# Performance work log

Measured on AMD Instinct MI355X. Metric: run time of the kernel, lower is better.

The kernel has to match this reference:

```python
import jax, jax.numpy as jnp
import numpy as np

N_NODES = 10000
N_EDGES = 160000
F_IN, D1, D2, D_OUT, K = 512, 512, 512, 256, 3


def _gcn_layer(x, row, col, w, W, b, n):
    # PyG GCNConv (improved=False): add self-loops with weight 1, sym norm.
    loop = jnp.arange(n)
    r = jnp.concatenate([row, loop])
    c = jnp.concatenate([col, loop])
    ww = jnp.concatenate([w, jnp.ones((n,), w.dtype)])
    deg = jax.ops.segment_sum(ww, c, num_segments=n)
    dinv = jnp.where(deg > 0, jax.lax.rsqrt(deg), 0.0)
    norm = dinv[r] * ww * dinv[c]              # [E+N]
    h = x @ W                                  # dense GEMM first (as PyG lin)
    out = jax.ops.segment_sum(norm[:, None] * h[r], c, num_segments=n)
    return out + b


def _cheb_layer(x, row, col, w, Wk, b, n):
    # PyG ChebConv, normalization='sym', lambda_max=2.0:
    # L_hat = 2L/lmax - I = -D^{-1/2} A D^{-1/2} (self-loops removed first).
    w0 = jnp.where(row == col, jnp.zeros((), w.dtype), w)  # remove self loops
    deg = jax.ops.segment_sum(w0, row, num_segments=n)
    dinv = jnp.where(deg > 0, jax.lax.rsqrt(deg), 0.0)
    norm = dinv[row] * w0 * dinv[col]          # [E]

    def lhat(z):  # L_hat @ z
        return -jax.ops.segment_sum(norm[:, None] * z[row], col, num_segments=n)

    Tx0 = x
    out = Tx0 @ Wk[0]
    Tx1 = lhat(x)
    out = out + Tx1 @ Wk[1]
    for k in range(2, Wk.shape[0]):            # static K, fine to unroll
        Tx2 = 2.0 * lhat(Tx1) - Tx0
        out = out + Tx2 @ Wk[k]
        Tx0, Tx1 = Tx1, Tx2
    return out + b


def setup_inputs() -> dict:
    key = jax.random.key(0)
    ks = jax.random.split(key, 9)
    x = jax.random.normal(ks[0], (N_NODES, F_IN), dtype=jnp.float32)
    edge_index = jax.random.randint(ks[1], (2, N_EDGES), 0, N_NODES, dtype=jnp.int64)
    edge_weight = jax.random.uniform(ks[2], (N_EDGES,), dtype=jnp.float32)
    s = lambda fan: 1.0 / np.sqrt(fan)
    W1 = jax.random.normal(ks[3], (F_IN, D1), dtype=jnp.float32) * s(F_IN)
    b1 = jnp.zeros((D1,), jnp.float32)
    W2 = jax.random.normal(ks[4], (D1, D2), dtype=jnp.float32) * s(D1)
    b2 = jnp.zeros((D2,), jnp.float32)
    Wc = jax.random.normal(ks[5], (K, D2, D_OUT), dtype=jnp.float32) * s(D2)
    bc = jnp.zeros((D_OUT,), jnp.float32)
    return {"x": x, "edge_index": edge_index, "edge_weight": edge_weight,
            "W1": W1, "b1": b1, "W2": W2, "b2": b2, "Wc": Wc, "bc": bc}


def reference(x, edge_index, edge_weight, W1, b1, W2, b2, Wc, bc):
    row, col = edge_index[0], edge_index[1]
    n = x.shape[0]
    h = jax.nn.celu(_gcn_layer(x, row, col, edge_weight, W1, b1, n))
    h = jax.nn.celu(_gcn_layer(h, row, col, edge_weight, W2, b2, n))
    h = jax.nn.celu(_cheb_layer(h, row, col, edge_weight, Wc, bc, n))
    return h
```

## Files before the change

kernel.cpp:

```cpp
#include <hip/hip_runtime.h>
#include <math.h>

#define N_NODES 10000
#define N_EDGES 160000
#define FDIM    512
#define DOUT    256
#define NCAT    768

typedef unsigned short ushort_t;
typedef unsigned int   uint_t;
typedef __attribute__((ext_vector_type(8))) short bf16x8;
typedef __attribute__((ext_vector_type(4))) float f32x4;

__device__ inline ushort_t f2bf(float f) {
    uint_t u = __float_as_uint(f);
    u += 0x7fffu + ((u >> 16) & 1u);
    return (ushort_t)(u >> 16);
}
__device__ inline void bf2f8(uint4 u, float* v) {
    v[0] = __uint_as_float(u.x << 16); v[1] = __uint_as_float(u.x & 0xffff0000u);
    v[2] = __uint_as_float(u.y << 16); v[3] = __uint_as_float(u.y & 0xffff0000u);
    v[4] = __uint_as_float(u.z << 16); v[5] = __uint_as_float(u.z & 0xffff0000u);
    v[6] = __uint_as_float(u.w << 16); v[7] = __uint_as_float(u.w & 0xffff0000u);
}
__device__ inline uint4 f2bf8v(const float* v) {
    uint4 u;
    u.x = (uint_t)f2bf(v[0]) | ((uint_t)f2bf(v[1]) << 16);
    u.y = (uint_t)f2bf(v[2]) | ((uint_t)f2bf(v[3]) << 16);
    u.z = (uint_t)f2bf(v[4]) | ((uint_t)f2bf(v[5]) << 16);
    u.w = (uint_t)f2bf(v[6]) | ((uint_t)f2bf(v[7]) << 16);
    return u;
}
__device__ inline void gld_lds16(const ushort_t* g, ushort_t* l) {
    __builtin_amdgcn_global_load_lds(
        (const __attribute__((address_space(1))) unsigned int*)g,
        (__attribute__((address_space(3))) unsigned int*)l,
        16, 0, 0);
}

#define EDGE_BLOCKS 625
#define XB_BLOCKS   5000

__global__ __launch_bounds__(256) void k_pre1(
    const int* __restrict__ row, const int* __restrict__ col,
    const float* __restrict__ w,
    float* deg_g, float* deg_c, int* counts,
    const float* __restrict__ x,  ushort_t* __restrict__ xb,
    const float* __restrict__ W1, ushort_t* __restrict__ W1t,
    const float* __restrict__ W2, ushort_t* __restrict__ W2t,
    const float* __restrict__ Wc, ushort_t* __restrict__ Wcatt)
{
    __shared__ float tile[64][65];
    int b = blockIdx.x;
    int tid = threadIdx.x;
    if (b < EDGE_BLOCKS) {
        int e = b * 256 + tid;
        if (e < N_EDGES) {
            int r = row[e], c = col[e];
            float wv = w[e];
            atomicAdd(&deg_g[c], wv);
            if (r != c) atomicAdd(&deg_c[r], wv);
            atomicAdd(&counts[c], 1);
        }
        return;
    }
    b -= EDGE_BLOCKS;
    if (b < XB_BLOCKS) {
        int t = b * 256 + tid;
        float4 v = *(const float4*)(x + (size_t)t * 4);
        uint2 p;
        p.x = (uint_t)f2bf(v.x) | ((uint_t)f2bf(v.y) << 16);
        p.y = (uint_t)f2bf(v.z) | ((uint_t)f2bf(v.w) << 16);
        *(uint2*)(xb + (size_t)t * 4) = p;
        return;
    }
    b -= XB_BLOCKS;
    const float* src; const float* src2 = nullptr;
    ushort_t* dst; int kt, ntG, srcld;
    if (b < 64) {
        kt = b >> 3; ntG = b & 7; srcld = FDIM;
        src = W1 + (size_t)(kt * 64) * FDIM + ntG * 64;
        dst = W1t;
    } else if (b < 128) {
        int bb = b - 64;
        kt = bb >> 3; ntG = bb & 7; srcld = FDIM;
        src = W2 + (size_t)(kt * 64) * FDIM + ntG * 64;
        dst = W2t;
    } else {
        int bb = b - 128;
        ntG = bb / 8; kt = bb % 8; srcld = DOUT;
        int s = ntG >> 2;
        int nl = (ntG & 3) * 64;
        if (s == 0) {
            src  = Wc + (size_t)(kt * 64) * DOUT + nl;
            src2 = Wc + (size_t)2 * FDIM * DOUT + (size_t)(kt * 64) * DOUT + nl;
        } else if (s == 1) {
            src  = Wc + (size_t)1 * FDIM * DOUT + (size_t)(kt * 64) * DOUT + nl;
        } else {
            src  = Wc + (size_t)2 * FDIM * DOUT + (size_t)(kt * 64) * DOUT + nl;
        }
        dst = Wcatt;
    }
    {
        int r = tid >> 2, c0 = (tid & 3) * 16;
        const float* sp = src + (size_t)r * srcld + c0;
#pragma unroll
        for (int q = 0; q < 4; ++q) {
            float4 a = *(const float4*)(sp + q * 4);
            if (src2) {
                float4 bsub = *(const float4*)(src2 + (size_t)r * srcld + c0 + q * 4);
                a.x -= bsub.x; a.y -= bsub.y; a.z -= bsub.z; a.w -= bsub.w;
            }
            tile[r][c0 + q * 4 + 0] = a.x;
            tile[r][c0 + q * 4 + 1] = a.y;
            tile[r][c0 + q * 4 + 2] = a.z;
            tile[r][c0 + q * 4 + 3] = a.w;
        }
    }
    __syncthreads();
    {
        int n = tid >> 2, k0 = (tid & 3) * 16;
        float v[16];
#pragma unroll
        for (int i = 0; i < 16; ++i) v[i] = tile[k0 + i][n];
        uint4 u0 = f2bf8v(v);
        uint4 u1 = f2bf8v(v + 8);
        ushort_t* dp = dst + (size_t)(ntG * 64 + n) * FDIM + kt * 64 + k0;
        *(uint4*)dp = u0;
        *(uint4*)(dp + 8) = u1;
    }
}

__global__ __launch_bounds__(256) void k_dinv_scan1(
    const float* __restrict__ deg_g, const float* __restrict__ deg_c,
    float* __restrict__ dinv_g, float* __restrict__ dinv_c,
    const int* __restrict__ counts, int* __restrict__ rp,
    int* __restrict__ part, int n)
{
    __shared__ int s[256];
    int tid = threadIdx.x;
    int i = blockIdx.x * 256 + tid;
    if (i < n) {
        dinv_g[i] = rsqrtf(deg_g[i] + 1.0f);
        float d = deg_c[i];
        dinv_c[i] = d > 0.f ? rsqrtf(d) : 0.f;
    }
    int v = (i < n) ? counts[i] : 0;
    s[tid] = v;
    __syncthreads();
    for (int o = 1; o < 256; o <<= 1) {
        int t = (tid >= o) ? s[tid - o] : 0;
        __syncthreads();
        s[tid] += t;
        __syncthreads();
    }
    if (i < n) rp[i] = s[tid] - v;
    if (tid == 255) part[blockIdx.x] = s[255];
}

__global__ __launch_bounds__(256) void k_scan23(int* __restrict__ rp,
                                                const int* __restrict__ part,
                                                int nb, int n) {
    __shared__ int soff[64];
    __shared__ int stot;
    int tid = threadIdx.x;
    if (tid < 64) {
        int v = (tid < nb) ? part[tid] : 0;
        int x = v;
        for (int o = 1; o < 64; o <<= 1) {
            int y = __shfl_up(x, o, 64);
            if (tid >= o) x += y;
        }
        soff[tid] = x - v;
        if (tid == 63) stot = x;
    }
    __syncthreads();
    int i = blockIdx.x * 256 + tid;
    if (i < n) rp[i] += soff[blockIdx.x];
    if (blockIdx.x == 0 && tid == 0) rp[n] = stot;
}

__global__ void k_fill(const int* __restrict__ row, const int* __restrict__ col,
                       const float* __restrict__ w,
                       const float* __restrict__ dinv_g, const float* __restrict__ dinv_c,
                       const int* __restrict__ rp, int* __restrict__ fill,
                       int2* __restrict__ eg, int2* __restrict__ ec, int E) {
    int e = blockIdx.x * blockDim.x + threadIdx.x;
    if (e >= E) return;
    int r = row[e], c = col[e];
    float wv = w[e];
    float ng = dinv_g[r] * wv * dinv_g[c];
    float w0 = (r == c) ? 0.f : wv;
    float nc = -(dinv_c[r] * w0 * dinv_c[c]);
    int pos = rp[c] + atomicAdd(&fill[c], 1);
    eg[pos] = make_int2(r, __float_as_int(ng));
    ec[pos] = make_int2(r, __float_as_int(nc));
}

__global__ __launch_bounds__(256) void k_mgemm(
    const ushort_t* __restrict__ A, int lda,
    const ushort_t* __restrict__ Bt, int ldb,
    int M, int K, int N, int nbx, int nby,
    ushort_t* __restrict__ outB)
{
    __shared__ ushort_t As[64 * 32];
    __shared__ ushort_t Bs[128 * 32];

    int id = blockIdx.x;
    int j = id & 7, t = id >> 3;
    int by = t % nby;
    int bx = (t / nby) * 8 + j;
    if (bx >= nbx) return;

    const int tid  = threadIdx.x;
    const int w    = tid >> 6;
    const int lane = tid & 63;
    const int l15  = lane & 15;
    const int quad = lane >> 4;
    const int bm = bx * 64, bn = by * 128;
    const int wm = (w & 1) * 32;
    const int wn = (w >> 1) * 64;

    const int sr = lane >> 2;
    const int sc = (lane & 3) * 8;
    int arow = min(bm + w * 16 + sr, M - 1);
    const ushort_t* ag = A + (size_t)arow * lda + sc;
    ushort_t* al = As + (w * 16 + sr) * 32 + sc;
    const ushort_t* bg0 = Bt + (size_t)(bn + w * 32 + sr) * ldb + sc;
    const ushort_t* bg1 = bg0 + (size_t)16 * ldb;
    ushort_t* bl0 = Bs + (w * 32 + sr) * 32 + sc;
    ushort_t* bl1 = bl0 + 16 * 32;

    f32x4 acc[2][4] = {};

    for (int k0 = 0; k0 < K; k0 += 32) {
        __syncthreads();
        gld_lds16(ag + k0, al);
        gld_lds16(bg0 + k0, bl0);
        gld_lds16(bg1 + k0, bl1);
        __syncthreads();
        bf16x8 af[2], bfr[4];
#pragma unroll
        for (int i = 0; i < 2; ++i)
            af[i] = *(const bf16x8*)(As + (wm + i * 16 + l15) * 32 + quad * 8);
#pragma unroll
        for (int jj = 0; jj < 4; ++jj)
            bfr[jj] = *(const bf16x8*)(Bs + (wn + jj * 16 + l15) * 32 + quad * 8);
#pragma unroll
        for (int i = 0; i < 2; ++i)
#pragma unroll
            for (int jj = 0; jj < 4; ++jj)
                acc[i][jj] = __builtin_amdgcn_mfma_f32_16x16x32_bf16(af[i], bfr[jj], acc[i][jj], 0, 0, 0);
    }

#pragma unroll
    for (int i = 0; i < 2; ++i) {
        int rowb = bm + wm + i * 16 + quad * 4;
#pragma unroll
        for (int jj = 0; jj < 4; ++jj) {
            int col = bn + wn + jj * 16 + l15;
#pragma unroll
            for (int r = 0; r < 4; ++r) {
                int rr = rowb + r;
                if (rr < M)
                    outB[(size_t)rr * N + col] = f2bf(acc[i][jj][r]);
            }
        }
    }
}

template<int SL>
__global__ __launch_bounds__(256) void k_sagg(
    const ushort_t* __restrict__ h, int hs, int hoff,
    const int2* __restrict__ er, const int* __restrict__ rp,
    const float* __restrict__ dinv_g,
    const ushort_t* __restrict__ other, int os, int ooff, float sB,
    const float* __restrict__ bias, float sA,
    ushort_t* __restrict__ outB, float* __restrict__ outF, int outs, int celu)
{
    const int id  = blockIdx.x;
    const int sl  = id % SL;
    const int tid = threadIdx.x;
    const int c   = (id / SL) * 32 + (tid >> 3);
    if (c >= N_NODES) return;
    const int f = sl * 64 + ((tid & 7) << 3);
    const ushort_t* hp = h + hoff + f;

    float acc[8] = {0.f, 0.f, 0.f, 0.f, 0.f, 0.f, 0.f, 0.f};
    int e = rp[c];
    const int e1 = rp[c + 1];
    for (; e + 4 <= e1; e += 4) {
        int2 p0 = er[e], p1 = er[e + 1], p2 = er[e + 2], p3 = er[e + 3];
        uint4 u0 = *(const uint4*)(hp + (size_t)p0.x * hs);
        uint4 u1 = *(const uint4*)(hp + (size_t)p1.x * hs);
        uint4 u2 = *(const uint4*)(hp + (size_t)p2.x * hs);
        uint4 u3 = *(const uint4*)(hp + (size_t)p3.x * hs);
        float n0 = __int_as_float(p0.y), n1 = __int_as_float(p1.y);
        float n2 = __int_as_float(p2.y), n3 = __int_as_float(p3.y);
        float v0[8], v1[8], v2[8], v3[8];
        bf2f8(u0, v0); bf2f8(u1, v1); bf2f8(u2, v2); bf2f8(u3, v3);
#pragma unroll
        for (int i = 0; i < 8; ++i) {
            acc[i] = fmaf(n0, v0[i], acc[i]);
            acc[i] = fmaf(n1, v1[i], acc[i]);
            acc[i] = fmaf(n2, v2[i], acc[i]);
            acc[i] = fmaf(n3, v3[i], acc[i]);
        }
    }
    for (; e < e1; ++e) {
        int2 p = er[e];
        uint4 u = *(const uint4*)(hp + (size_t)p.x * hs);
        float nv = __int_as_float(p.y);
        float v[8]; bf2f8(u, v);
#pragma unroll
        for (int i = 0; i < 8; ++i) acc[i] = fmaf(nv, v[i], acc[i]);
    }

    if (dinv_g) {
        float dv = dinv_g[c];
        float d2 = dv * dv;
        uint4 u = *(const uint4*)(hp + (size_t)c * hs);
        float v[8]; bf2f8(u, v);
#pragma unroll
        for (int i = 0; i < 8; ++i) acc[i] = fmaf(d2, v[i], acc[i]);
    }
    float r[8];
#pragma unroll
    for (int i = 0; i < 8; ++i) r[i] = sA * acc[i];
    if (other) {
        uint4 u = *(const uint4*)(other + (size_t)c * os + ooff + f);
        float o[8]; bf2f8(u, o);
#pragma unroll
        for (int i = 0; i < 8; ++i) r[i] = fmaf(sB, o[i], r[i]);
    }
    if (bias) {
#pragma unroll
        for (int i = 0; i < 8; ++i) r[i] += bias[f + i];
    }
    if (celu) {
#pragma unroll
        for (int i = 0; i < 8; ++i) r[i] = r[i] > 0.f ? r[i] : expm1f(r[i]);
    }
    if (outF) {
        float* op = outF + (size_t)c * outs + f;
        *(float4*)op       = make_float4(r[0], r[1], r[2], r[3]);
        *(float4*)(op + 4) = make_float4(r[4], r[5], r[6], r[7]);
    } else {
        *(uint4*)(outB + (size_t)c * outs + f) = f2bf8v(r);
    }
}


extern "C" void kernel_launch(void* const* d_in, const int* in_sizes, int n_in,
                              void* d_out, int out_size, void* d_ws, size_t ws_size,
                              hipStream_t stream) {
    const float* x  = (const float*)d_in[0];
    const int*   ei = (const int*)d_in[1];
    const float* ew = (const float*)d_in[2];
    const float* W1 = (const float*)d_in[3];
    const float* b1 = (const float*)d_in[4];
    const float* W2 = (const float*)d_in[5];
    const float* b2 = (const float*)d_in[6];
    const float* Wc = (const float*)d_in[7];
    const float* bc = (const float*)d_in[8];
    float* out = (float*)d_out;

    const int* row = ei;
    const int* col = ei + N_EDGES;

    char* ws = (char*)d_ws;
    size_t off = 0;
    auto alloc = [&](size_t bytes) -> void* {
        void* p = ws + off;
        off += (bytes + 255) & ~(size_t)255;
        return p;
    };
    ushort_t* xb    = (ushort_t*)alloc((size_t)N_NODES * FDIM * 2);
    ushort_t* bufA  = (ushort_t*)alloc((size_t)N_NODES * FDIM * 2);
    ushort_t* bufB  = (ushort_t*)alloc((size_t)N_NODES * FDIM * 2);
    ushort_t* Y     = (ushort_t*)alloc((size_t)N_NODES * NCAT * 2);
    ushort_t* P     = (ushort_t*)alloc((size_t)N_NODES * DOUT * 2);
    ushort_t* W1t   = (ushort_t*)alloc((size_t)FDIM * FDIM * 2);
    ushort_t* W2t   = (ushort_t*)alloc((size_t)FDIM * FDIM * 2);
    ushort_t* Wcatt = (ushort_t*)alloc((size_t)NCAT * FDIM * 2);
    size_t zs = off;
    float* deg_g  = (float*)alloc((size_t)N_NODES * 4);
    float* deg_c  = (float*)alloc((size_t)N_NODES * 4);
    int*   counts = (int*)alloc((size_t)N_NODES * 4);
    int*   fillb  = (int*)alloc((size_t)N_NODES * 4);
    size_t ze = off;
    float* dinv_g = (float*)alloc((size_t)N_NODES * 4);
    float* dinv_c = (float*)alloc((size_t)N_NODES * 4);
    int*   rp     = (int*)alloc((size_t)(N_NODES + 1) * 4);
    int*   part   = (int*)alloc(64 * 4);
    int2*  eg     = (int2*)alloc((size_t)N_EDGES * 8);
    int2*  ec     = (int2*)alloc((size_t)N_EDGES * 8);

    const int TB = 256;
    dim3 edgeGrid((N_EDGES + TB - 1) / TB);
    int nScanB = (N_NODES + 255) / 256;

    hipMemsetAsync(ws + zs, 0, ze - zs, stream);
    k_pre1<<<EDGE_BLOCKS + XB_BLOCKS + 224, 256, 0, stream>>>(
        row, col, ew, deg_g, deg_c, counts,
        x, xb, W1, W1t, W2, W2t, Wc, Wcatt);
    k_dinv_scan1<<<nScanB, 256, 0, stream>>>(deg_g, deg_c, dinv_g, dinv_c, counts, rp, part, N_NODES);
    k_scan23<<<nScanB, 256, 0, stream>>>(rp, part, nScanB, N_NODES);
    k_fill<<<edgeGrid, TB, 0, stream>>>(row, col, ew, dinv_g, dinv_c, rp, fillb, eg, ec, N_EDGES);

    auto mgemm = [&](const ushort_t* A, const ushort_t* Bt, int N, ushort_t* oB) {
        int nbx = (N_NODES + 63) / 64, nby = N / 128;
        int G = 8 * (((nbx + 7) / 8) * nby);
        k_mgemm<<<G, 256, 0, stream>>>(A, FDIM, Bt, FDIM, N_NODES, FDIM, N, nbx, nby, oB);
    };
    int g8 = ((N_NODES + 31) / 32) * 8;
    int g4 = ((N_NODES + 31) / 32) * 4;

    mgemm(xb, W1t, FDIM, bufA);
    k_sagg<8><<<g8, 256, 0, stream>>>(bufA, FDIM, 0, eg, rp, dinv_g,
                                      (const ushort_t*)nullptr, 0, 0, 0.f,
                                      b1, 1.f, bufB, (float*)nullptr, FDIM, 1);
    mgemm(bufB, W2t, FDIM, bufA);
    k_sagg<8><<<g8, 256, 0, stream>>>(bufA, FDIM, 0, eg, rp, dinv_g,
                                      (const ushort_t*)nullptr, 0, 0, 0.f,
                                      b2, 1.f, bufB, (float*)nullptr, FDIM, 1);
    mgemm(bufB, Wcatt, NCAT, Y);
    k_sagg<4><<<g4, 256, 0, stream>>>(Y, NCAT, 2 * DOUT, ec, rp,
                                      (const float*)nullptr,
                                      Y, NCAT, DOUT, 1.f,
                                      (const float*)nullptr, 2.f,
                                      P, (float*)nullptr, DOUT, 0);
    k_sagg<4><<<g4, 256, 0, stream>>>(P, DOUT, 0, ec, rp,
                                      (const float*)nullptr,
                                      Y, NCAT, 0, 1.f,
                                      bc, 1.f,
                                      (ushort_t*)nullptr, out, DOUT, 1);
}
```

Before: 240.1 us.

## Fuse all stages into one persistent kernel with software grid barriers

Replaces the sequence of eleven kernel launches with a single persistent kernel. A grid-stride loop runs each stage's virtual blocks, and an atomic-counter grid barrier separates the stages. The aim is to remove per-launch overhead and inter-kernel drain gaps. In exchange the grid is capped by occupancy (at most 1024 blocks, launch bounds of 3 blocks per CU), and the kernel carries a union shared-memory footprint and extra register pressure. Barrier spin costs and relying on all blocks being co-resident add risk.

```diff
diff --git a/kernel.cpp b/kernel.cpp
--- a/kernel.cpp
+++ b/kernel.cpp
@@ -6,6 +6,17 @@
 #define FDIM    512
 #define DOUT    256
 #define NCAT    768
+
+#define EDGE_BLOCKS 625
+#define XB_BLOCKS   5000
+#define W_BLOCKS    224
+#define PRE1_TASKS  (EDGE_BLOCKS + XB_BLOCKS + W_BLOCKS)
+#define SCAN_BLOCKS 40
+#define FILL_BLOCKS 625
+#define NV_SAGG8    (313 * 8)
+#define NV_SAGG4    (313 * 4)
+#define G_GEMM1     640
+#define G_GEMM3     960
 
 typedef unsigned short ushort_t;
 typedef unsigned int   uint_t;
@@ -38,40 +49,57 @@
         16, 0, 0);
 }
 
-#define EDGE_BLOCKS 625
-#define XB_BLOCKS   5000
-
-__global__ __launch_bounds__(256) void k_pre1(
-    const int* __restrict__ row, const int* __restrict__ col,
-    const float* __restrict__ w,
-    float* deg_g, float* deg_c, int* counts,
-    const float* __restrict__ x,  ushort_t* __restrict__ xb,
-    const float* __restrict__ W1, ushort_t* __restrict__ W1t,
-    const float* __restrict__ W2, ushort_t* __restrict__ W2t,
-    const float* __restrict__ Wc, ushort_t* __restrict__ Wcatt)
-{
-    __shared__ float tile[64][65];
-    int b = blockIdx.x;
-    int tid = threadIdx.x;
+struct MegaParams {
+    const float* x; const int* row; const int* col; const float* ew;
+    const float* W1; const float* b1; const float* W2; const float* b2;
+    const float* Wc; const float* bc; float* out;
+    ushort_t* xb; ushort_t* bufA; ushort_t* bufB; ushort_t* Y; ushort_t* P;
+    ushort_t* W1t; ushort_t* W2t; ushort_t* Wcatt;
+    float* deg_g; float* deg_c; int* counts; int* fillb; unsigned* bar;
+    float* dinv_g; float* dinv_c; int* rp; int* part;
+    int2* eg; int2* ec;
+};
+
+union SMem {
+    float tile[64][65];
+    struct { ushort_t As[64 * 32]; ushort_t Bs[128 * 32]; } g;
+    int scan[256];
+    struct { int soff[64]; int stot; } s23;
+};
+
+__device__ inline void gsync(unsigned* bar, int nb) {
+    __syncthreads();
+    if (threadIdx.x == 0) {
+        __threadfence();
+        unsigned old = atomicAdd(bar, 1u);
+        unsigned target = (old / (unsigned)nb + 1u) * (unsigned)nb;
+        while (__hip_atomic_load(bar, __ATOMIC_RELAXED, __HIP_MEMORY_SCOPE_AGENT) < target)
+            __builtin_amdgcn_s_sleep(2);
+        __threadfence();
+    }
+    __syncthreads();
+}
+
+__device__ void d_pre1(const MegaParams& p, int b, int tid, SMem& sm) {
     if (b < EDGE_BLOCKS) {
         int e = b * 256 + tid;
         if (e < N_EDGES) {
-            int r = row[e], c = col[e];
-            float wv = w[e];
-            atomicAdd(&deg_g[c], wv);
-            if (r != c) atomicAdd(&deg_c[r], wv);
-            atomicAdd(&counts[c], 1);
+            int r = p.row[e], c = p.col[e];
+            float wv = p.ew[e];
+            atomicAdd(&p.deg_g[c], wv);
+            if (r != c) atomicAdd(&p.deg_c[r], wv);
+            atomicAdd(&p.counts[c], 1);
         }
         return;
     }
     b -= EDGE_BLOCKS;
     if (b < XB_BLOCKS) {
         int t = b * 256 + tid;
-        float4 v = *(const float4*)(x + (size_t)t * 4);
-        uint2 p;
-        p.x = (uint_t)f2bf(v.x) | ((uint_t)f2bf(v.y) << 16);
-        p.y = (uint_t)f2bf(v.z) | ((uint_t)f2bf(v.w) << 16);
-        *(uint2*)(xb + (size_t)t * 4) = p;
+        float4 v = *(const float4*)(p.x + (size_t)t * 4);
+        uint2 q;
+        q.x = (uint_t)f2bf(v.x) | ((uint_t)f2bf(v.y) << 16);
+        q.y = (uint_t)f2bf(v.z) | ((uint_t)f2bf(v.w) << 16);
+        *(uint2*)(p.xb + (size_t)t * 4) = q;
         return;
     }
     b -= XB_BLOCKS;
@@ -79,28 +107,29 @@
     ushort_t* dst; int kt, ntG, srcld;
     if (b < 64) {
         kt = b >> 3; ntG = b & 7; srcld = FDIM;
-        src = W1 + (size_t)(kt * 64) * FDIM + ntG * 64;
-        dst = W1t;
+        src = p.W1 + (size_t)(kt * 64) * FDIM + ntG * 64;
+        dst = p.W1t;
     } else if (b < 128) {
         int bb = b - 64;
         kt = bb >> 3; ntG = bb & 7; srcld = FDIM;
-        src = W2 + (size_t)(kt * 64) * FDIM + ntG * 64;
-        dst = W2t;
+        src = p.W2 + (size_t)(kt * 64) * FDIM + ntG * 64;
+        dst = p.W2t;
     } else {
         int bb = b - 128;
         ntG = bb / 8; kt = bb % 8; srcld = DOUT;
         int s = ntG >> 2;
         int nl = (ntG & 3) * 64;
         if (s == 0) {
-            src  = Wc + (size_t)(kt * 64) * DOUT + nl;
-            src2 = Wc + (size_t)2 * FDIM * DOUT + (size_t)(kt * 64) * DOUT + nl;
+            src  = p.Wc + (size_t)(kt * 64) * DOUT + nl;
+            src2 = p.Wc + (size_t)2 * FDIM * DOUT + (size_t)(kt * 64) * DOUT + nl;
         } else if (s == 1) {
-            src  = Wc + (size_t)1 * FDIM * DOUT + (size_t)(kt * 64) * DOUT + nl;
+            src  = p.Wc + (size_t)1 * FDIM * DOUT + (size_t)(kt * 64) * DOUT + nl;
         } else {
-            src  = Wc + (size_t)2 * FDIM * DOUT + (size_t)(kt * 64) * DOUT + nl;
-        }
-        dst = Wcatt;
-    }
+            src  = p.Wc + (size_t)2 * FDIM * DOUT + (size_t)(kt * 64) * DOUT + nl;
+        }
+        dst = p.Wcatt;
+    }
+    __syncthreads();
     {
         int r = tid >> 2, c0 = (tid & 3) * 16;
         const float* sp = src + (size_t)r * srcld + c0;
@@ -111,10 +140,10 @@
                 float4 bsub = *(const float4*)(src2 + (size_t)r * srcld + c0 + q * 4);
                 a.x -= bsub.x; a.y -= bsub.y; a.z -= bsub.z; a.w -= bsub.w;
             }
-            tile[r][c0 + q * 4 + 0] = a.x;
-            tile[r][c0 + q * 4 + 1] = a.y;
-            tile[r][c0 + q * 4 + 2] = a.z;
-            tile[r][c0 + q * 4 + 3] = a.w;
+            sm.tile[r][c0 + q * 4 + 0] = a.x;
+            sm.tile[r][c0 + q * 4 + 1] = a.y;
+            sm.tile[r][c0 + q * 4 + 2] = a.z;
+            sm.tile[r][c0 + q * 4 + 3] = a.w;
         }
     }
     __syncthreads();
@@ -122,7 +151,7 @@
         int n = tid >> 2, k0 = (tid & 3) * 16;
         float v[16];
 #pragma unroll
-        for (int i = 0; i < 16; ++i) v[i] = tile[k0 + i][n];
+        for (int i = 0; i < 16; ++i) v[i] = sm.tile[k0 + i][n];
         uint4 u0 = f2bf8v(v);
         uint4 u1 = f2bf8v(v + 8);
         ushort_t* dp = dst + (size_t)(ntG * 64 + n) * FDIM + kt * 64 + k0;
@@ -131,88 +160,66 @@
     }
 }
 
-__global__ __launch_bounds__(256) void k_dinv_scan1(
-    const float* __restrict__ deg_g, const float* __restrict__ deg_c,
-    float* __restrict__ dinv_g, float* __restrict__ dinv_c,
-    const int* __restrict__ counts, int* __restrict__ rp,
-    int* __restrict__ part, int n)
-{
-    __shared__ int s[256];
-    int tid = threadIdx.x;
-    int i = blockIdx.x * 256 + tid;
-    if (i < n) {
-        dinv_g[i] = rsqrtf(deg_g[i] + 1.0f);
-        float d = deg_c[i];
-        dinv_c[i] = d > 0.f ? rsqrtf(d) : 0.f;
-    }
-    int v = (i < n) ? counts[i] : 0;
-    s[tid] = v;
+__device__ void d_scan1(const MegaParams& p, int vb, int tid, SMem& sm) {
+    int i = vb * 256 + tid;
+    if (i < N_NODES) {
+        p.dinv_g[i] = rsqrtf(p.deg_g[i] + 1.0f);
+        float d = p.deg_c[i];
+        p.dinv_c[i] = d > 0.f ? rsqrtf(d) : 0.f;
+    }
+    int v = (i < N_NODES) ? p.counts[i] : 0;
+    sm.scan[tid] = v;
     __syncthreads();
     for (int o = 1; o < 256; o <<= 1) {
-        int t = (tid >= o) ? s[tid - o] : 0;
+        int t = (tid >= o) ? sm.scan[tid - o] : 0;
         __syncthreads();
-        s[tid] += t;
+        sm.scan[tid] += t;
         __syncthreads();
     }
-    if (i < n) rp[i] = s[tid] - v;
-    if (tid == 255) part[blockIdx.x] = s[255];
-}
-
-__global__ __launch_bounds__(256) void k_scan23(int* __restrict__ rp,
-                                                const int* __restrict__ part,
-                                                int nb, int n) {
-    __shared__ int soff[64];
-    __shared__ int stot;
-    int tid = threadIdx.x;
+    if (i < N_NODES) p.rp[i] = sm.scan[tid] - v;
+    if (tid == 255) p.part[vb] = sm.scan[255];
+}
+
+__device__ void d_scan23(const MegaParams& p, int vb, int tid, SMem& sm) {
     if (tid < 64) {
-        int v = (tid < nb) ? part[tid] : 0;
+        int v = (tid < SCAN_BLOCKS) ? p.part[tid] : 0;
         int x = v;
         for (int o = 1; o < 64; o <<= 1) {
             int y = __shfl_up(x, o, 64);
             if (tid >= o) x += y;
         }
-        soff[tid] = x - v;
-        if (tid == 63) stot = x;
-    }
-    __syncthreads();
-    int i = blockIdx.x * 256 + tid;
-    if (i < n) rp[i] += soff[blockIdx.x];
-    if (blockIdx.x == 0 && tid == 0) rp[n] = stot;
-}
-
-__global__ void k_fill(const int* __restrict__ row, const int* __restrict__ col,
-                       const float* __restrict__ w,
-                       const float* __restrict__ dinv_g, const float* __restrict__ dinv_c,
-                       const int* __restrict__ rp, int* __restrict__ fill,
-                       int2* __restrict__ eg, int2* __restrict__ ec, int E) {
-    int e = blockIdx.x * blockDim.x + threadIdx.x;
-    if (e >= E) return;
-    int r = row[e], c = col[e];
-    float wv = w[e];
-    float ng = dinv_g[r] * wv * dinv_g[c];
+        sm.s23.soff[tid] = x - v;
+        if (tid == 63) sm.s23.stot = x;
+    }
+    __syncthreads();
+    int i = vb * 256 + tid;
+    if (i < N_NODES) p.rp[i] += sm.s23.soff[vb];
+    if (vb == 0 && tid == 0) p.rp[N_NODES] = sm.s23.stot;
+}
+
+__device__ void d_fill(const MegaParams& p, int vb, int tid) {
+    int e = vb * 256 + tid;
+    if (e >= N_EDGES) return;
+    int r = p.row[e], c = p.col[e];
+    float wv = p.ew[e];
+    float ng = p.dinv_g[r] * wv * p.dinv_g[c];
     float w0 = (r == c) ? 0.f : wv;
-    float nc = -(dinv_c[r] * w0 * dinv_c[c]);
-    int pos = rp[c] + atomicAdd(&fill[c], 1);
-    eg[pos] = make_int2(r, __float_as_int(ng));
-    ec[pos] = make_int2(r, __float_as_int(nc));
-}
-
-__global__ __launch_bounds__(256) void k_mgemm(
-    const ushort_t* __restrict__ A, int lda,
-    const ushort_t* __restrict__ Bt, int ldb,
-    int M, int K, int N, int nbx, int nby,
-    ushort_t* __restrict__ outB)
+    float nc = -(p.dinv_c[r] * w0 * p.dinv_c[c]);
+    int pos = p.rp[c] + atomicAdd(&p.fillb[c], 1);
+    p.eg[pos] = make_int2(r, __float_as_int(ng));
+    p.ec[pos] = make_int2(r, __float_as_int(nc));
+}
+
+__device__ void d_gemm(SMem& sm, const ushort_t* __restrict__ A,
+                       const ushort_t* __restrict__ Bt, int N,
+                       int nbx, int nby, int vb, int tid,
+                       ushort_t* __restrict__ outB)
 {
-    __shared__ ushort_t As[64 * 32];
-    __shared__ ushort_t Bs[128 * 32];
-
-    int id = blockIdx.x;
-    int j = id & 7, t = id >> 3;
+    int j = vb & 7, t = vb >> 3;
     int by = t % nby;
     int bx = (t / nby) * 8 + j;
     if (bx >= nbx) return;
 
-    const int tid  = threadIdx.x;
     const int w    = tid >> 6;
     const int lane = tid & 63;
     const int l15  = lane & 15;
@@ -223,17 +230,17 @@
 
     const int sr = lane >> 2;
     const int sc = (lane & 3) * 8;
-    int arow = min(bm + w * 16 + sr, M - 1);
-    const ushort_t* ag = A + (size_t)arow * lda + sc;
-    ushort_t* al = As + (w * 16 + sr) * 32 + sc;
-    const ushort_t* bg0 = Bt + (size_t)(bn + w * 32 + sr) * ldb + sc;
-    const ushort_t* bg1 = bg0 + (size_t)16 * ldb;
-    ushort_t* bl0 = Bs + (w * 32 + sr) * 32 + sc;
+    int arow = min(bm + w * 16 + sr, N_NODES - 1);
+    const ushort_t* ag = A + (size_t)arow * FDIM + sc;
+    ushort_t* al = sm.g.As + (w * 16 + sr) * 32 + sc;
+    const ushort_t* bg0 = Bt + (size_t)(bn + w * 32 + sr) * FDIM + sc;
+    const ushort_t* bg1 = bg0 + (size_t)16 * FDIM;
+    ushort_t* bl0 = sm.g.Bs + (w * 32 + sr) * 32 + sc;
     ushort_t* bl1 = bl0 + 16 * 32;
 
     f32x4 acc[2][4] = {};
 
-    for (int k0 = 0; k0 < K; k0 += 32) {
+    for (int k0 = 0; k0 < FDIM; k0 += 32) {
         __syncthreads();
         gld_lds16(ag + k0, al);
         gld_lds16(bg0 + k0, bl0);
@@ -242,10 +249,10 @@
         bf16x8 af[2], bfr[4];
 #pragma unroll
         for (int i = 0; i < 2; ++i)
-            af[i] = *(const bf16x8*)(As + (wm + i * 16 + l15) * 32 + quad * 8);
+            af[i] = *(const bf16x8*)(sm.g.As + (wm + i * 16 + l15) * 32 + quad * 8);
 #pragma unroll
         for (int jj = 0; jj < 4; ++jj)
-            bfr[jj] = *(const bf16x8*)(Bs + (wn + jj * 16 + l15) * 32 + quad * 8);
+            bfr[jj] = *(const bf16x8*)(sm.g.Bs + (wn + jj * 16 + l15) * 32 + quad * 8);
 #pragma unroll
         for (int i = 0; i < 2; ++i)
 #pragma unroll
@@ -262,7 +269,7 @@
 #pragma unroll
             for (int r = 0; r < 4; ++r) {
                 int rr = rowb + r;
-                if (rr < M)
+                if (rr < N_NODES)
                     outB[(size_t)rr * N + col] = f2bf(acc[i][jj][r]);
             }
         }
@@ -270,25 +277,22 @@
 }
 
 template<int SL>
-__global__ __launch_bounds__(256) void k_sagg(
+__device__ void d_sagg(const MegaParams& p, int vb, int tid,
     const ushort_t* __restrict__ h, int hs, int hoff,
-    const int2* __restrict__ er, const int* __restrict__ rp,
-    const float* __restrict__ dinv_g,
+    const int2* __restrict__ er, const float* __restrict__ dinv_g,
     const ushort_t* __restrict__ other, int os, int ooff, float sB,
     const float* __restrict__ bias, float sA,
     ushort_t* __restrict__ outB, float* __restrict__ outF, int outs, int celu)
 {
-    const int id  = blockIdx.x;
-    const int sl  = id % SL;
-    const int tid = threadIdx.x;
-    const int c   = (id / SL) * 32 + (tid >> 3);
+    const int sl = vb % SL;
+    const int c  = (vb / SL) * 32 + (tid >> 3);
     if (c >= N_NODES) return;
     const int f = sl * 64 + ((tid & 7) << 3);
     const ushort_t* hp = h + hoff + f;
 
     float acc[8] = {0.f, 0.f, 0.f, 0.f, 0.f, 0.f, 0.f, 0.f};
-    int e = rp[c];
-    const int e1 = rp[c + 1];
+    int e = p.rp[c];
+    const int e1 = p.rp[c + 1];
     for (; e + 4 <= e1; e += 4) {
         int2 p0 = er[e], p1 = er[e + 1], p2 = er[e + 2], p3 = er[e + 3];
         uint4 u0 = *(const uint4*)(hp + (size_t)p0.x * hs);
@@ -308,9 +312,9 @@
         }
     }
     for (; e < e1; ++e) {
-        int2 p = er[e];
-        uint4 u = *(const uint4*)(hp + (size_t)p.x * hs);
-        float nv = __int_as_float(p.y);
+        int2 pe = er[e];
+        uint4 u = *(const uint4*)(hp + (size_t)pe.x * hs);
+        float nv = __int_as_float(pe.y);
         float v[8]; bf2f8(u, v);
 #pragma unroll
         for (int i = 0; i < 8; ++i) acc[i] = fmaf(nv, v[i], acc[i]);
@@ -348,6 +352,52 @@
     } else {
         *(uint4*)(outB + (size_t)c * outs + f) = f2bf8v(r);
     }
+}
+
+__global__ __launch_bounds__(256, 3) void k_mega(MegaParams p) {
+    __shared__ SMem sm;
+    const int tid = threadIdx.x;
+    const int b0  = blockIdx.x;
+    const int NB  = gridDim.x;
+
+    for (int vb = b0; vb < PRE1_TASKS; vb += NB) d_pre1(p, vb, tid, sm);
+    gsync(p.bar, NB);
+    for (int vb = b0; vb < SCAN_BLOCKS; vb += NB) d_scan1(p, vb, tid, sm);
+    gsync(p.bar, NB);
+    for (int vb = b0; vb < SCAN_BLOCKS; vb += NB) d_scan23(p, vb, tid, sm);
+    gsync(p.bar, NB);
+    for (int vb = b0; vb < FILL_BLOCKS; vb += NB) d_fill(p, vb, tid);
+    gsync(p.bar, NB);
+    for (int vb = b0; vb < G_GEMM1; vb += NB)
+        d_gemm(sm, p.xb, p.W1t, FDIM, 157, 4, vb, tid, p.bufA);
+    gsync(p.bar, NB);
+    for (int vb = b0; vb < NV_SAGG8; vb += NB)
+        d_sagg<8>(p, vb, tid, p.bufA, FDIM, 0, p.eg, p.dinv_g,
+                  (const ushort_t*)nullptr, 0, 0, 0.f, p.b1, 1.f,
+                  p.bufB, (float*)nullptr, FDIM, 1);
+    gsync(p.bar, NB);
+    for (int vb = b0; vb < G_GEMM1; vb += NB)
+        d_gemm(sm, p.bufB, p.W2t, FDIM, 157, 4, vb, tid, p.bufA);
+    gsync(p.bar, NB);
+    for (int vb = b0; vb < NV_SAGG8; vb += NB)
+        d_sagg<8>(p, vb, tid, p.bufA, FDIM, 0, p.eg, p.dinv_g,
+                  (const ushort_t*)nullptr, 0, 0, 0.f, p.b2, 1.f,
+                  p.bufB, (float*)nullptr, FDIM, 1);
+    gsync(p.bar, NB);
+    for (int vb = b0; vb < G_GEMM3; vb += NB)
+        d_gemm(sm, p.bufB, p.Wcatt, NCAT, 157, 6, vb, tid, p.Y);
+    gsync(p.bar, NB);
+    for (int vb = b0; vb < NV_SAGG4; vb += NB)
+        d_sagg<4>(p, vb, tid, p.Y, NCAT, 2 * DOUT, p.ec,
+                  (const float*)nullptr, p.Y, NCAT, DOUT, 1.f,
+                  (const float*)nullptr, 2.f,
+                  p.P, (float*)nullptr, DOUT, 0);
+    gsync(p.bar, NB);
+    for (int vb = b0; vb < NV_SAGG4; vb += NB)
+        d_sagg<4>(p, vb, tid, p.P, DOUT, 0, p.ec,
+                  (const float*)nullptr, p.Y, NCAT, 0, 1.f,
+                  p.bc, 1.f,
+                  (ushort_t*)nullptr, p.out, DOUT, 1);
 }
 
 
@@ -365,9 +415,6 @@
     const float* bc = (const float*)d_in[8];
     float* out = (float*)d_out;
 
-    const int* row = ei;
-    const int* col = ei + N_EDGES;
-
     char* ws = (char*)d_ws;
     size_t off = 0;
     auto alloc = [&](size_t bytes) -> void* {
@@ -375,64 +422,43 @@
         off += (bytes + 255) & ~(size_t)255;
         return p;
     };
-    ushort_t* xb    = (ushort_t*)alloc((size_t)N_NODES * FDIM * 2);
-    ushort_t* bufA  = (ushort_t*)alloc((size_t)N_NODES * FDIM * 2);
-    ushort_t* bufB  = (ushort_t*)alloc((size_t)N_NODES * FDIM * 2);
-    ushort_t* Y     = (ushort_t*)alloc((size_t)N_NODES * NCAT * 2);
-    ushort_t* P     = (ushort_t*)alloc((size_t)N_NODES * DOUT * 2);
-    ushort_t* W1t   = (ushort_t*)alloc((size_t)FDIM * FDIM * 2);
-    ushort_t* W2t   = (ushort_t*)alloc((size_t)FDIM * FDIM * 2);
-    ushort_t* Wcatt = (ushort_t*)alloc((size_t)NCAT * FDIM * 2);
+    MegaParams P;
+    P.x = x; P.row = ei; P.col = ei + N_EDGES; P.ew = ew;
+    P.W1 = W1; P.b1 = b1; P.W2 = W2; P.b2 = b2; P.Wc = Wc; P.bc = bc;
+    P.out = out;
+
+    P.xb    = (ushort_t*)alloc((size_t)N_NODES * FDIM * 2);
+    P.bufA  = (ushort_t*)alloc((size_t)N_NODES * FDIM * 2);
+    P.bufB  = (ushort_t*)alloc((size_t)N_NODES * FDIM * 2);
+    P.Y     = (ushort_t*)alloc((size_t)N_NODES * NCAT * 2);
+    P.P     = (ushort_t*)alloc((size_t)N_NODES * DOUT * 2);
+    P.W1t   = (ushort_t*)alloc((size_t)FDIM * FDIM * 2);
+    P.W2t   = (ushort_t*)alloc((size_t)FDIM * FDIM * 2);
+    P.Wcatt = (ushort_t*)alloc((size_t)NCAT * FDIM * 2);
     size_t zs = off;
-    float* deg_g  = (float*)alloc((size_t)N_NODES * 4);
-    float* deg_c  = (float*)alloc((size_t)N_NODES * 4);
-    int*   counts = (int*)alloc((size_t)N_NODES * 4);
-    int*   fillb  = (int*)alloc((size_t)N_NODES * 4);
+    P.deg_g  = (float*)alloc((size_t)N_NODES * 4);
+    P.deg_c  = (float*)alloc((size_t)N_NODES * 4);
+    P.counts = (int*)alloc((size_t)N_NODES * 4);
+    P.fillb  = (int*)alloc((size_t)N_NODES * 4);
+    P.bar    = (unsigned*)alloc(256);
     size_t ze = off;
-    float* dinv_g = (float*)alloc((size_t)N_NODES * 4);
-    float* dinv_c = (float*)alloc((size_t)N_NODES * 4);
-    int*   rp     = (int*)alloc((size_t)(N_NODES + 1) * 4);
-    int*   part   = (int*)alloc(64 * 4);
-    int2*  eg     = (int2*)alloc((size_t)N_EDGES * 8);
-    int2*  ec     = (int2*)alloc((size_t)N_EDGES * 8);
-
-    const int TB = 256;
-    dim3 edgeGrid((N_EDGES + TB - 1) / TB);
-    int nScanB = (N_NODES + 255) / 256;
+    P.dinv_g = (float*)alloc((size_t)N_NODES * 4);
+    P.dinv_c = (float*)alloc((size_t)N_NODES * 4);
+    P.rp     = (int*)alloc((size_t)(N_NODES + 1) * 4);
+    P.part   = (int*)alloc(64 * 4);
+    P.eg     = (int2*)alloc((size_t)N_EDGES * 8);
+    P.ec     = (int2*)alloc((size_t)N_EDGES * 8);
+
+    static int g_grid = 0;
+    if (g_grid == 0) {
+        int occ = 0;
+        (void)hipOccupancyMaxActiveBlocksPerMultiprocessor(&occ, k_mega, 256, 0);
+        if (occ < 1) occ = 1;
+        long g = (long)occ * 256;
+        if (g > 1024) g = 1024;
+        g_grid = (int)g;
+    }
 
     hipMemsetAsync(ws + zs, 0, ze - zs, stream);
-    k_pre1<<<EDGE_BLOCKS + XB_BLOCKS + 224, 256, 0, stream>>>(
-        row, col, ew, deg_g, deg_c, counts,
-        x, xb, W1, W1t, W2, W2t, Wc, Wcatt);
-    k_dinv_scan1<<<nScanB, 256, 0, stream>>>(deg_g, deg_c, dinv_g, dinv_c, counts, rp, part, N_NODES);
-    k_scan23<<<nScanB, 256, 0, stream>>>(rp, part, nScanB, N_NODES);
-    k_fill<<<edgeGrid, TB, 0, stream>>>(row, col, ew, dinv_g, dinv_c, rp, fillb, eg, ec, N_EDGES);
-
-    auto mgemm = [&](const ushort_t* A, const ushort_t* Bt, int N, ushort_t* oB) {
-        int nbx = (N_NODES + 63) / 64, nby = N / 128;
-        int G = 8 * (((nbx + 7) / 8) * nby);
-        k_mgemm<<<G, 256, 0, stream>>>(A, FDIM, Bt, FDIM, N_NODES, FDIM, N, nbx, nby, oB);
-    };
-    int g8 = ((N_NODES + 31) / 32) * 8;
-    int g4 = ((N_NODES + 31) / 32) * 4;
-
-    mgemm(xb, W1t, FDIM, bufA);
-    k_sagg<8><<<g8, 256, 0, stream>>>(bufA, FDIM, 0, eg, rp, dinv_g,
-                                      (const ushort_t*)nullptr, 0, 0, 0.f,
-                                      b1, 1.f, bufB, (float*)nullptr, FDIM, 1);
-    mgemm(bufB, W2t, FDIM, bufA);
-    k_sagg<8><<<g8, 256, 0, stream>>>(bufA, FDIM, 0, eg, rp, dinv_g,
-                                      (const ushort_t*)nullptr, 0, 0, 0.f,
-                                      b2, 1.f, bufB, (float*)nullptr, FDIM, 1);
-    mgemm(bufB, Wcatt, NCAT, Y);
-    k_sagg<4><<<g4, 256, 0, stream>>>(Y, NCAT, 2 * DOUT, ec, rp,
-                                      (const float*)nullptr,
-                                      Y, NCAT, DOUT, 1.f,
-                                      (const float*)nullptr, 2.f,
-                                      P, (float*)nullptr, DOUT, 0);
-    k_sagg<4><<<g4, 256, 0, stream>>>(P, DOUT, 0, ec, rp,
-                                      (const float*)nullptr,
-                                      Y, NCAT, 0, 1.f,
-                                      bc, 1.f,
-                                      (ushort_t*)nullptr, out, DOUT, 1);
-}
+    k_mega<<<g_grid, 256, 0, stream>>>(P);
+}
```

Measured after the change: 872.0 us. 263% more time.

## Merge scan into one block and fuse edge fill with first GEMM

Applied to the files above, without the earlier changes.

Replaces the two-kernel prefix scan (block scan plus partial-sum fixup) with a single 1024-thread kernel that scans all node counts and computes the inverse degrees. Merges the CSR edge-fill kernel and the first layer's GEMM into one launch, with block IDs split between edge-fill and GEMM tiles so the two independent jobs run concurrently. This removes two kernel launches and lets the small fill work overlap the GEMM. The single-block scan runs serially on one CU, and the fused GEMM path is a separate copy of the generic GEMM with hardcoded sizes.

```diff
diff --git a/kernel.cpp b/kernel.cpp
--- a/kernel.cpp
+++ b/kernel.cpp
@@ -40,6 +40,8 @@
 
 #define EDGE_BLOCKS 625
 #define XB_BLOCKS   5000
+#define FILL_BLOCKS 625
+#define G_GEMM1     640
 
 __global__ __launch_bounds__(256) void k_pre1(
     const int* __restrict__ row, const int* __restrict__ col,
@@ -131,70 +133,139 @@
     }
 }
 
-__global__ __launch_bounds__(256) void k_dinv_scan1(
+__global__ __launch_bounds__(1024) void k_scanfull(
     const float* __restrict__ deg_g, const float* __restrict__ deg_c,
     float* __restrict__ dinv_g, float* __restrict__ dinv_c,
-    const int* __restrict__ counts, int* __restrict__ rp,
-    int* __restrict__ part, int n)
+    const int* __restrict__ counts, int* __restrict__ rp)
 {
-    __shared__ int s[256];
-    int tid = threadIdx.x;
-    int i = blockIdx.x * 256 + tid;
-    if (i < n) {
-        dinv_g[i] = rsqrtf(deg_g[i] + 1.0f);
-        float d = deg_c[i];
-        dinv_c[i] = d > 0.f ? rsqrtf(d) : 0.f;
-    }
-    int v = (i < n) ? counts[i] : 0;
-    s[tid] = v;
+    __shared__ int wsum[16];
+    const int tid  = threadIdx.x;
+    const int base = tid * 10;
+    int loc[10]; int sum = 0;
+#pragma unroll
+    for (int j = 0; j < 10; ++j) {
+        int i = base + j;
+        int v = (i < N_NODES) ? counts[i] : 0;
+        loc[j] = sum; sum += v;
+        if (i < N_NODES) {
+            dinv_g[i] = rsqrtf(deg_g[i] + 1.0f);
+            float d = deg_c[i];
+            dinv_c[i] = d > 0.f ? rsqrtf(d) : 0.f;
+        }
+    }
+    const int lane = tid & 63, wid = tid >> 6;
+    int x = sum;
+    for (int o = 1; o < 64; o <<= 1) {
+        int y = __shfl_up(x, o, 64);
+        if (lane >= o) x += y;
+    }
+    if (lane == 63) wsum[wid] = x;
     __syncthreads();
-    for (int o = 1; o < 256; o <<= 1) {
-        int t = (tid >= o) ? s[tid - o] : 0;
+    if (wid == 0) {
+        int v = (lane < 16) ? wsum[lane] : 0;
+        int y = v;
+        for (int o = 1; o < 16; o <<= 1) {
+            int z = __shfl_up(y, o, 64);
+            if (lane >= o) y += z;
+        }
+        if (lane < 16) wsum[lane] = y - v;
+    }
+    __syncthreads();
+    const int off = wsum[wid] + (x - sum);
+#pragma unroll
+    for (int j = 0; j < 10; ++j) {
+        int i = base + j;
+        if (i <= N_NODES) rp[i] = off + loc[j];
+    }
+}
+
+__global__ __launch_bounds__(256) void k_fillgemm(
+    const int* __restrict__ row, const int* __restrict__ col,
+    const float* __restrict__ w,
+    const float* __restrict__ dinv_g, const float* __restrict__ dinv_c,
+    const int* __restrict__ rp, int* __restrict__ fillb,
+    int2* __restrict__ eg, int2* __restrict__ ec,
+    const ushort_t* __restrict__ A, const ushort_t* __restrict__ Bt,
+    ushort_t* __restrict__ outB)
+{
+    __shared__ ushort_t As[64 * 32];
+    __shared__ ushort_t Bs[128 * 32];
+    const int tid = threadIdx.x;
+    int id = blockIdx.x;
+
+    if (id < FILL_BLOCKS) {
+        int e = id * 256 + tid;
+        if (e >= N_EDGES) return;
+        int r = row[e], c = col[e];
+        float wv = w[e];
+        float ng = dinv_g[r] * wv * dinv_g[c];
+        float w0 = (r == c) ? 0.f : wv;
+        float nc = -(dinv_c[r] * w0 * dinv_c[c]);
+        int pos = rp[c] + atomicAdd(&fillb[c], 1);
+        eg[pos] = make_int2(r, __float_as_int(ng));
+        ec[pos] = make_int2(r, __float_as_int(nc));
+        return;
+    }
+
+    int vb = id - FILL_BLOCKS;
+    int j = vb & 7, t = vb >> 3;
+    int by = t % 4;
+    int bx = (t / 4) * 8 + j;
+    if (bx >= 157) return;
+
+    const int w4   = tid >> 6;
+    const int lane = tid & 63;
+    const int l15  = lane & 15;
+    const int quad = lane >> 4;
+    const int bm = bx * 64, bn = by * 128;
+    const int wm = (w4 & 1) * 32;
+    const int wn = (w4 >> 1) * 64;
+
+    const int sr = lane >> 2;
+    const int sc = (lane & 3) * 8;
+    int arow = min(bm + w4 * 16 + sr, N_NODES - 1);
+    const ushort_t* ag = A + (size_t)arow * FDIM + sc;
+    ushort_t* al = As + (w4 * 16 + sr) * 32 + sc;
+    const ushort_t* bg0 = Bt + (size_t)(bn + w4 * 32 + sr) * FDIM + sc;
+    const ushort_t* bg1 = bg0 + (size_t)16 * FDIM;
+    ushort_t* bl0 = Bs + (w4 * 32 + sr) * 32 + sc;
+    ushort_t* bl1 = bl0 + 16 * 32;
+
+    f32x4 acc[2][4] = {};
+
+    for (int k0 = 0; k0 < FDIM; k0 += 32) {
         __syncthreads();
-        s[tid] += t;
+        gld_lds16(ag + k0, al);
+        gld_lds16(bg0 + k0, bl0);
+        gld_lds16(bg1 + k0, bl1);
         __syncthreads();
-    }
-    if (i < n) rp[i] = s[tid] - v;
-    if (tid == 255) part[blockIdx.x] = s[255];
-}
-
-__global__ __launch_bounds__(256) void k_scan23(int* __restrict__ rp,
-                                                const int* __restrict__ part,
-                                                int nb, int n) {
-    __shared__ int soff[64];
-    __shared__ int stot;
-    int tid = threadIdx.x;
-    if (tid < 64) {
-        int v = (tid < nb) ? part[tid] : 0;
-        int x = v;
-        for (int o = 1; o < 64; o <<= 1) {
-            int y = __shfl_up(x, o, 64);
-            if (tid >= o) x += y;
-        }
-        soff[tid] = x - v;
-        if (tid == 63) stot = x;
-    }
-    __syncthreads();
-    int i = blockIdx.x * 256 + tid;
-    if (i < n) rp[i] += soff[blockIdx.x];
-    if (blockIdx.x == 0 && tid == 0) rp[n] = stot;
-}
-
-__global__ void k_fill(const int* __restrict__ row, const int* __restrict__ col,
-                       const float* __restrict__ w,
-                       const float* __restrict__ dinv_g, const float* __restrict__ dinv_c,
-                       const int* __restrict__ rp, int* __restrict__ fill,
-                       int2* __restrict__ eg, int2* __restrict__ ec, int E) {
-    int e = blockIdx.x * blockDim.x + threadIdx.x;
-    if (e >= E) return;
-    int r = row[e], c = col[e];
-    float wv = w[e];
-    float ng = dinv_g[r] * wv * dinv_g[c];
-    float w0 = (r == c) ? 0.f : wv;
-    float nc = -(dinv_c[r] * w0 * dinv_c[c]);
-    int pos = rp[c] + atomicAdd(&fill[c], 1);
-    eg[pos] = make_int2(r, __float_as_int(ng));
-    ec[pos] = make_int2(r, __float_as_int(nc));
+        bf16x8 af[2], bfr[4];
+#pragma unroll
+        for (int i = 0; i < 2; ++i)
+            af[i] = *(const bf16x8*)(As + (wm + i * 16 + l15) * 32 + quad * 8);
+#pragma unroll
+        for (int jj = 0; jj < 4; ++jj)
+            bfr[jj] = *(const bf16x8*)(Bs + (wn + jj * 16 + l15) * 32 + quad * 8);
+#pragma unroll
+        for (int i = 0; i < 2; ++i)
+#pragma unroll
+            for (int jj = 0; jj < 4; ++jj)
+                acc[i][jj] = __builtin_amdgcn_mfma_f32_16x16x32_bf16(af[i], bfr[jj], acc[i][jj], 0, 0, 0);
+    }
+#pragma unroll
+    for (int i = 0; i < 2; ++i) {
+        int rowb = bm + wm + i * 16 + quad * 4;
+#pragma unroll
+        for (int jj = 0; jj < 4; ++jj) {
+            int colc = bn + wn + jj * 16 + l15;
+#pragma unroll
+            for (int r = 0; r < 4; ++r) {
+                int rr = rowb + r;
+                if (rr < N_NODES)
+                    outB[(size_t)rr * FDIM + colc] = f2bf(acc[i][jj][r]);
+            }
+        }
+    }
 }
 
 __global__ __launch_bounds__(256) void k_mgemm(
@@ -392,21 +463,16 @@
     float* dinv_g = (float*)alloc((size_t)N_NODES * 4);
     float* dinv_c = (float*)alloc((size_t)N_NODES * 4);
     int*   rp     = (int*)alloc((size_t)(N_NODES + 1) * 4);
-    int*   part   = (int*)alloc(64 * 4);
     int2*  eg     = (int2*)alloc((size_t)N_EDGES * 8);
     int2*  ec     = (int2*)alloc((size_t)N_EDGES * 8);
-
-    const int TB = 256;
-    dim3 edgeGrid((N_EDGES + TB - 1) / TB);
-    int nScanB = (N_NODES + 255) / 256;
 
     hipMemsetAsync(ws + zs, 0, ze - zs, stream);
     k_pre1<<<EDGE_BLOCKS + XB_BLOCKS + 224, 256, 0, stream>>>(
         row, col, ew, deg_g, deg_c, counts,
         x, xb, W1, W1t, W2, W2t, Wc, Wcatt);
-    k_dinv_scan1<<<nScanB, 256, 0, stream>>>(deg_g, deg_c, dinv_g, dinv_c, counts, rp, part, N_NODES);
-    k_scan23<<<nScanB, 256, 0, stream>>>(rp, part, nScanB, N_NODES);
-    k_fill<<<edgeGrid, TB, 0, stream>>>(row, col, ew, dinv_g, dinv_c, rp, fillb, eg, ec, N_EDGES);
+    k_scanfull<<<1, 1024, 0, stream>>>(deg_g, deg_c, dinv_g, dinv_c, counts, rp);
+    k_fillgemm<<<FILL_BLOCKS + G_GEMM1, 256, 0, stream>>>(
+        row, col, ew, dinv_g, dinv_c, rp, fillb, eg, ec, xb, W1t, bufA);
 
     auto mgemm = [&](const ushort_t* A, const ushort_t* Bt, int N, ushort_t* oB) {
         int nbx = (N_NODES + 63) / 64, nby = N / 128;
@@ -416,7 +482,6 @@
     int g8 = ((N_NODES + 31) / 32) * 8;
     int g4 = ((N_NODES + 31) / 32) * 4;
 
-    mgemm(xb, W1t, FDIM, bufA);
     k_sagg<8><<<g8, 256, 0, stream>>>(bufA, FDIM, 0, eg, rp, dinv_g,
                                       (const ushort_t*)nullptr, 0, 0, 0.f,
                                       b1, 1.f, bufB, (float*)nullptr, FDIM, 1);
```

Result: slower. 246.8 us (+2.8%).
